# Performance work log

Measured on AMD Instinct MI355X. Metric: run time of the kernel, lower is better.

The kernel has to match this reference:

```python
import jax, jax.numpy as jnp
import numpy as np

FP8_MAX = 448.0  # torch.finfo(torch.float8_e4m3fn).max
FP8_MIN = -448.0
EPS = 1e-12


def fp8_quantize(x):
    """Scalar (per-tensor) dynamic fp8 e4m3 quantization, matching fp8_quantize(scalar=True).
    Returns fp8-rounded values (stored as float32) and the reciprocal scale (float32)."""
    amax = jnp.clip(jnp.max(jnp.abs(x)), EPS, None)
    scale = FP8_MAX / amax
    q = jnp.clip(x * scale, FP8_MIN, FP8_MAX)
    q = q.astype(jnp.float8_e4m3fn).astype(jnp.float32)  # rounding to fp8 grid
    return q, (1.0 / scale).astype(jnp.float32)


def setup_inputs() -> dict:
    key = jax.random.key(0)
    k_in, k_w, k_b = jax.random.split(key, 3)
    M, K, N = 16384, 2048, 2048
    input = jax.random.normal(k_in, (M, K), dtype=jnp.float32)
    weight = jax.random.normal(k_w, (N, K), dtype=jnp.float32) * 0.02
    # from_unquant: quantize weight once at init
    qweight, w_scale = fp8_quantize(weight)
    bias = jax.random.normal(k_b, (N,), dtype=jnp.float32) * 0.01
    return {"input": input, "qweight": qweight, "w_scale": w_scale, "bias": bias}


def reference(input, qweight, w_scale, bias):
    # dynamic per-tensor fp8 quantization of the activation
    qinput, a_scale = fp8_quantize(input)  # [M, K], scalar
    # torch._scaled_mm(qinput, qweight.t(), scale_a, scale_b, bias):
    #   out = (A_fp8 @ B_fp8) * scale_a * scale_b + bias, in out_dtype
    out = jnp.matmul(qinput, qweight.T)  # [M, N]
    out = out * (a_scale * w_scale) + bias[None, :]
    return out.astype(jnp.float32)
```

## Files before the change

### kernel.cpp

```cpp
#include <hip/hip_runtime.h>

typedef float f32x4 __attribute__((ext_vector_type(4)));
typedef int   i32x4 __attribute__((ext_vector_type(4)));
typedef int   i32x8 __attribute__((ext_vector_type(8)));

#define FP8MAX 448.0f
#define AMAX_BLOCKS 2048
#define WQ_BLOCKS 512
#define QA_BLOCKS 2048


__device__ __forceinline__ unsigned pack_fp8_exact(float4 v) {
    int r = __builtin_amdgcn_cvt_pk_fp8_f32(v.x, v.y, 0, false);
    return (unsigned)__builtin_amdgcn_cvt_pk_fp8_f32(v.z, v.w, r, true);
}

__global__ __launch_bounds__(256) void amax_and_wquant(
    const float4* __restrict__ x, float* __restrict__ partial, int n4,
    const float4* __restrict__ w, uint4* __restrict__ qw, int n16w) {
    if (blockIdx.x < AMAX_BLOCKS) {
        float m0 = 0.0f, m1 = 0.0f;
        int stride = AMAX_BLOCKS * 256;
        int i = blockIdx.x * 256 + threadIdx.x;
        for (; i + stride < n4; i += 2 * stride) {
            float4 a = x[i];
            float4 b = x[i + stride];
            m0 = fmaxf(m0, fmaxf(fmaxf(fabsf(a.x), fabsf(a.y)), fmaxf(fabsf(a.z), fabsf(a.w))));
            m1 = fmaxf(m1, fmaxf(fmaxf(fabsf(b.x), fabsf(b.y)), fmaxf(fabsf(b.z), fabsf(b.w))));
        }
        if (i < n4) {
            float4 a = x[i];
            m0 = fmaxf(m0, fmaxf(fmaxf(fabsf(a.x), fabsf(a.y)), fmaxf(fabsf(a.z), fabsf(a.w))));
        }
        float m = fmaxf(m0, m1);
#pragma unroll
        for (int off = 32; off > 0; off >>= 1)
            m = fmaxf(m, __shfl_down(m, off, 64));
        __shared__ float ws[4];
        if ((threadIdx.x & 63) == 0) ws[threadIdx.x >> 6] = m;
        __syncthreads();
        if (threadIdx.x == 0)
            partial[blockIdx.x] = fmaxf(fmaxf(ws[0], ws[1]), fmaxf(ws[2], ws[3]));
    } else {
        int stride = WQ_BLOCKS * 256;
        for (int i = (blockIdx.x - AMAX_BLOCKS) * 256 + threadIdx.x; i < n16w; i += stride) {
            uint4 r;
            r.x = pack_fp8_exact(w[i * 4 + 0]);
            r.y = pack_fp8_exact(w[i * 4 + 1]);
            r.z = pack_fp8_exact(w[i * 4 + 2]);
            r.w = pack_fp8_exact(w[i * 4 + 3]);
            qw[i] = r;
        }
    }
}


__device__ __forceinline__ float reduce_partials(const float* __restrict__ partial) {
    float m = 0.0f;
#pragma unroll
    for (int j = 0; j < AMAX_BLOCKS / 256; ++j)
        m = fmaxf(m, partial[threadIdx.x + j * 256]);
#pragma unroll
    for (int off = 32; off > 0; off >>= 1)
        m = fmaxf(m, __shfl_down(m, off, 64));
    __shared__ float ws[4];
    if ((threadIdx.x & 63) == 0) ws[threadIdx.x >> 6] = m;
    __syncthreads();
    return fmaxf(fmaxf(ws[0], ws[1]), fmaxf(ws[2], ws[3]));
}

__device__ __forceinline__ unsigned pack_fp8_clip(float4 v, float s) {
    float a = fminf(fmaxf(v.x * s, -FP8MAX), FP8MAX);
    float b = fminf(fmaxf(v.y * s, -FP8MAX), FP8MAX);
    float c = fminf(fmaxf(v.z * s, -FP8MAX), FP8MAX);
    float d = fminf(fmaxf(v.w * s, -FP8MAX), FP8MAX);
    int r = __builtin_amdgcn_cvt_pk_fp8_f32(a, b, 0, false);
    r = __builtin_amdgcn_cvt_pk_fp8_f32(c, d, r, true);
    return (unsigned)r;
}

__global__ __launch_bounds__(256) void quant_act(
    const float4* __restrict__ x, uint4* __restrict__ q,
    const float* __restrict__ partial, unsigned* __restrict__ amax_bits, int n16) {
    float amax = fmaxf(reduce_partials(partial), 1e-12f);
    if (blockIdx.x == 0 && threadIdx.x == 0)
        *amax_bits = __float_as_uint(amax);
    float s = FP8MAX / amax;
    int stride = QA_BLOCKS * 256;
    for (int i = blockIdx.x * 256 + threadIdx.x; i < n16; i += stride) {
        uint4 r;
        r.x = pack_fp8_clip(x[i * 4 + 0], s);
        r.y = pack_fp8_clip(x[i * 4 + 1], s);
        r.z = pack_fp8_clip(x[i * 4 + 2], s);
        r.w = pack_fp8_clip(x[i * 4 + 3], s);
        q[i] = r;
    }
}


__global__ __launch_bounds__(256) void gemm_fp8_mx(
    const unsigned char* __restrict__ Aq,
    const unsigned char* __restrict__ Bq,
    const unsigned* __restrict__ amax_bits,
    const float* __restrict__ w_scale_p,
    const float* __restrict__ bias,
    float* __restrict__ C,
    int M, int N, int K) {
    __shared__ unsigned char lA[128 * 128];
    __shared__ unsigned char lB[128 * 128];

    const int tid = threadIdx.x;
    const int lane = tid & 63;
    const int wave = tid >> 6;

    const int bn = blockIdx.x;
    const int bm = blockIdx.y;
    const int row0 = bm * 128;
    const int col0 = bn * 128;

    const int wm = wave >> 1;
    const int wn = wave & 1;
    const int m_base = wm * 64;
    const int n_base = wn * 64;

    const int lane_lo = lane & 15;
    const int h = lane >> 4;
    const int c0 = 2 * h;
    const int c1 = 2 * h + 1;

    f32x4 acc[4][4];
#pragma unroll
    for (int i = 0; i < 4; ++i)
#pragma unroll
        for (int j = 0; j < 4; ++j)
            acc[i][j] = (f32x4){0.f, 0.f, 0.f, 0.f};

    union frag8 { i32x8 v; i32x4 half[2]; };

    for (int k0 = 0; k0 < K; k0 += 128) {
#pragma unroll
        for (int it = 0; it < 4; ++it) {
            int chunk = tid + it * 256;
            int r = chunk >> 3;
            int cpos = chunk & 7;
            int csrc = cpos ^ (r & 7);
            const unsigned char* gA = Aq + (size_t)(row0 + r) * K + (k0 + csrc * 16);
            const unsigned char* gB = Bq + (size_t)(col0 + r) * K + (k0 + csrc * 16);
            __builtin_amdgcn_global_load_lds(
                (const __attribute__((address_space(1))) void*)gA,
                (__attribute__((address_space(3))) void*)(lA + chunk * 16), 16, 0, 0);
            __builtin_amdgcn_global_load_lds(
                (const __attribute__((address_space(1))) void*)gB,
                (__attribute__((address_space(3))) void*)(lB + chunk * 16), 16, 0, 0);
        }
        __syncthreads();

        frag8 af[4], bf[4];
#pragma unroll
        for (int i = 0; i < 4; ++i) {
            int m = m_base + i * 16 + lane_lo;
            int p0 = c0 ^ (m & 7);
            int p1 = c1 ^ (m & 7);
            af[i].half[0] = *(const i32x4*)(lA + m * 128 + p0 * 16);
            af[i].half[1] = *(const i32x4*)(lA + m * 128 + p1 * 16);
        }
#pragma unroll
        for (int j = 0; j < 4; ++j) {
            int n = n_base + j * 16 + lane_lo;
            int p0 = c0 ^ (n & 7);
            int p1 = c1 ^ (n & 7);
            bf[j].half[0] = *(const i32x4*)(lB + n * 128 + p0 * 16);
            bf[j].half[1] = *(const i32x4*)(lB + n * 128 + p1 * 16);
        }
#pragma unroll
        for (int i = 0; i < 4; ++i)
#pragma unroll
            for (int j = 0; j < 4; ++j)
                acc[i][j] = __builtin_amdgcn_mfma_scale_f32_16x16x128_f8f6f4(
                    af[i].v, bf[j].v, acc[i][j],
                    0, 0,
                    0, 0x7F7F7F7F,
                    0, 0x7F7F7F7F);
        __syncthreads();
    }

    float amax = fmaxf(__uint_as_float(*amax_bits), 1e-12f);
    float scale = FP8MAX / amax;
    float a_scale = 1.0f / scale;
    float s = a_scale * w_scale_p[0];

    const int lane_hi = lane >> 4;
#pragma unroll
    for (int i = 0; i < 4; ++i) {
#pragma unroll
        for (int j = 0; j < 4; ++j) {
            int col = col0 + n_base + j * 16 + lane_lo;
            float bv = bias[col];
#pragma unroll
            for (int r = 0; r < 4; ++r) {
                int row = row0 + m_base + i * 16 + lane_hi * 4 + r;
                C[(size_t)row * N + col] = acc[i][j][r] * s + bv;
            }
        }
    }
}


extern "C" void kernel_launch(void* const* d_in, const int* in_sizes, int n_in,
                              void* d_out, int out_size, void* d_ws, size_t ws_size,
                              hipStream_t stream) {
    const float* input   = (const float*)d_in[0];
    const float* qweight = (const float*)d_in[1];
    const float* w_scale = (const float*)d_in[2];
    const float* bias    = (const float*)d_in[3];
    float* out = (float*)d_out;

    const int N = in_sizes[3];
    const int K = in_sizes[1] / N;
    const int M = in_sizes[0] / K;

    unsigned* amax_bits = (unsigned*)d_ws;
    float* partial = (float*)((char*)d_ws + 256);
    unsigned char* qA = (unsigned char*)d_ws + 16384;
    unsigned char* qW = qA + (size_t)M * K;

    const int n4a  = (M / 4) * K;
    const int n16w = (N / 4) * K / 4;
    hipLaunchKernelGGL(amax_and_wquant, dim3(AMAX_BLOCKS + WQ_BLOCKS), dim3(256), 0, stream,
                       (const float4*)input, partial, n4a,
                       (const float4*)qweight, (uint4*)qW, n16w);

    const int n16a = n4a / 4;
    hipLaunchKernelGGL(quant_act, dim3(QA_BLOCKS), dim3(256), 0, stream,
                       (const float4*)input, (uint4*)qA, partial, amax_bits, n16a);

    hipLaunchKernelGGL(gemm_fp8_mx, dim3(N / 128, M / 128), dim3(256), 0, stream,
                       qA, qW, amax_bits, w_scale, bias, out, M, N, K);
}
```

Before: 325.7 us.

## Use 256x256 tiles with 8 waves and double-buffered LDS prefetch in FP8 GEMM

The GEMM tile grows from 128x128 with 4 waves to 256x256 with 8 waves, and each wave now computes a 128x64 sub-tile. LDS is double-buffered so the next K-tile's global-to-LDS loads are interleaved with the MFMA phases of the current tile, with barriers and s_setprio around the MFMA bursts. This aims to hide global load latency and halve the global traffic per FLOP. In exchange it raises LDS use to 128 KB per block and doubles the accumulator registers, which limits occupancy to about one block per CU.

```diff
diff --git a/kernel.cpp b/kernel.cpp
--- a/kernel.cpp
+++ b/kernel.cpp
@@ -98,7 +98,7 @@
 }
 
 
-__global__ __launch_bounds__(256) void gemm_fp8_mx(
+__global__ __launch_bounds__(512) void gemm_fp8_mx2(
     const unsigned char* __restrict__ Aq,
     const unsigned char* __restrict__ Bq,
     const unsigned* __restrict__ amax_bits,
@@ -106,8 +106,8 @@
     const float* __restrict__ bias,
     float* __restrict__ C,
     int M, int N, int K) {
-    __shared__ unsigned char lA[128 * 128];
-    __shared__ unsigned char lB[128 * 128];
+    __shared__ unsigned char lA[2][256 * 128];
+    __shared__ unsigned char lB[2][256 * 128];
 
     const int tid = threadIdx.x;
     const int lane = tid & 63;
@@ -115,12 +115,12 @@
 
     const int bn = blockIdx.x;
     const int bm = blockIdx.y;
-    const int row0 = bm * 128;
-    const int col0 = bn * 128;
-
-    const int wm = wave >> 1;
-    const int wn = wave & 1;
-    const int m_base = wm * 64;
+    const int row0 = bm * 256;
+    const int col0 = bn * 256;
+
+    const int wm = wave >> 2;
+    const int wn = wave & 3;
+    const int m_base = wm * 128;
     const int n_base = wn * 64;
 
     const int lane_lo = lane & 15;
@@ -128,60 +128,98 @@
     const int c0 = 2 * h;
     const int c1 = 2 * h + 1;
 
-    f32x4 acc[4][4];
-#pragma unroll
-    for (int i = 0; i < 4; ++i)
+    const int s_r    = tid >> 3;
+    const int s_cpos = tid & 7;
+
+    f32x4 acc[8][4];
+#pragma unroll
+    for (int i = 0; i < 8; ++i)
 #pragma unroll
         for (int j = 0; j < 4; ++j)
             acc[i][j] = (f32x4){0.f, 0.f, 0.f, 0.f};
 
     union frag8 { i32x8 v; i32x4 half[2]; };
 
-    for (int k0 = 0; k0 < K; k0 += 128) {
-#pragma unroll
-        for (int it = 0; it < 4; ++it) {
-            int chunk = tid + it * 256;
-            int r = chunk >> 3;
-            int cpos = chunk & 7;
-            int csrc = cpos ^ (r & 7);
-            const unsigned char* gA = Aq + (size_t)(row0 + r) * K + (k0 + csrc * 16);
-            const unsigned char* gB = Bq + (size_t)(col0 + r) * K + (k0 + csrc * 16);
-            __builtin_amdgcn_global_load_lds(
-                (const __attribute__((address_space(1))) void*)gA,
-                (__attribute__((address_space(3))) void*)(lA + chunk * 16), 16, 0, 0);
-            __builtin_amdgcn_global_load_lds(
-                (const __attribute__((address_space(1))) void*)gB,
-                (__attribute__((address_space(3))) void*)(lB + chunk * 16), 16, 0, 0);
-        }
-        __syncthreads();
-
-        frag8 af[4], bf[4];
-#pragma unroll
-        for (int i = 0; i < 4; ++i) {
-            int m = m_base + i * 16 + lane_lo;
-            int p0 = c0 ^ (m & 7);
-            int p1 = c1 ^ (m & 7);
-            af[i].half[0] = *(const i32x4*)(lA + m * 128 + p0 * 16);
-            af[i].half[1] = *(const i32x4*)(lA + m * 128 + p1 * 16);
-        }
-#pragma unroll
-        for (int j = 0; j < 4; ++j) {
-            int n = n_base + j * 16 + lane_lo;
-            int p0 = c0 ^ (n & 7);
-            int p1 = c1 ^ (n & 7);
-            bf[j].half[0] = *(const i32x4*)(lB + n * 128 + p0 * 16);
-            bf[j].half[1] = *(const i32x4*)(lB + n * 128 + p1 * 16);
-        }
-#pragma unroll
-        for (int i = 0; i < 4; ++i)
+#define STAGE_PAIR(BUFI, KT, IT)                                                        \
+    {                                                                                   \
+        int r_ = s_r + (IT) * 64;                                                       \
+        int csrc_ = s_cpos ^ (r_ & 7);                                                  \
+        int ldst_ = (r_ * 8 + s_cpos) * 16;                                             \
+        const unsigned char* gA_ = Aq + (size_t)(row0 + r_) * K + ((KT) * 128 + csrc_ * 16); \
+        const unsigned char* gB_ = Bq + (size_t)(col0 + r_) * K + ((KT) * 128 + csrc_ * 16); \
+        __builtin_amdgcn_global_load_lds(                                               \
+            (const __attribute__((address_space(1))) void*)gA_,                         \
+            (__attribute__((address_space(3))) void*)(&lA[BUFI][0] + ldst_), 16, 0, 0); \
+        __builtin_amdgcn_global_load_lds(                                               \
+            (const __attribute__((address_space(1))) void*)gB_,                         \
+            (__attribute__((address_space(3))) void*)(&lB[BUFI][0] + ldst_), 16, 0, 0); \
+    }
+
+#pragma unroll
+    for (int it = 0; it < 4; ++it)
+        STAGE_PAIR(0, 0, it)
+    asm volatile("s_waitcnt vmcnt(0)" ::: "memory");
+    __builtin_amdgcn_s_barrier();
+
+    const int NT = K >> 7;
+    int buf = 0;
+    for (int t = 0; t < NT; ++t) {
+        const unsigned char* cA = &lA[buf][0];
+        const unsigned char* cB = &lB[buf][0];
+        const int nbuf = buf ^ 1;
+        const bool pf = (t + 1 < NT);
+
+        frag8 bfr[4];
+#pragma unroll
+        for (int p = 0; p < 4; ++p) {
+            if (p == 0) {
+#pragma unroll
+                for (int j = 0; j < 4; ++j) {
+                    int n = n_base + j * 16 + lane_lo;
+                    int p0 = c0 ^ (n & 7);
+                    int p1 = c1 ^ (n & 7);
+                    bfr[j].half[0] = *(const i32x4*)(cB + n * 128 + p0 * 16);
+                    bfr[j].half[1] = *(const i32x4*)(cB + n * 128 + p1 * 16);
+                }
+            }
+            frag8 a0, a1;
+            {
+                int m = m_base + (2 * p) * 16 + lane_lo;
+                int p0 = c0 ^ (m & 7);
+                int p1 = c1 ^ (m & 7);
+                a0.half[0] = *(const i32x4*)(cA + m * 128 + p0 * 16);
+                a0.half[1] = *(const i32x4*)(cA + m * 128 + p1 * 16);
+            }
+            {
+                int m = m_base + (2 * p + 1) * 16 + lane_lo;
+                int p0 = c0 ^ (m & 7);
+                int p1 = c1 ^ (m & 7);
+                a1.half[0] = *(const i32x4*)(cA + m * 128 + p0 * 16);
+                a1.half[1] = *(const i32x4*)(cA + m * 128 + p1 * 16);
+            }
+            if (pf)
+                STAGE_PAIR(nbuf, t + 1, p)
+
+            __builtin_amdgcn_s_barrier();
+
+            __builtin_amdgcn_s_setprio(1);
 #pragma unroll
             for (int j = 0; j < 4; ++j)
-                acc[i][j] = __builtin_amdgcn_mfma_scale_f32_16x16x128_f8f6f4(
-                    af[i].v, bf[j].v, acc[i][j],
-                    0, 0,
-                    0, 0x7F7F7F7F,
-                    0, 0x7F7F7F7F);
-        __syncthreads();
+                acc[2 * p][j] = __builtin_amdgcn_mfma_scale_f32_16x16x128_f8f6f4(
+                    a0.v, bfr[j].v, acc[2 * p][j],
+                    0, 0, 0, 0x7F7F7F7F, 0, 0x7F7F7F7F);
+#pragma unroll
+            for (int j = 0; j < 4; ++j)
+                acc[2 * p + 1][j] = __builtin_amdgcn_mfma_scale_f32_16x16x128_f8f6f4(
+                    a1.v, bfr[j].v, acc[2 * p + 1][j],
+                    0, 0, 0, 0x7F7F7F7F, 0, 0x7F7F7F7F);
+            __builtin_amdgcn_s_setprio(0);
+
+            if (p == 3 && pf)
+                asm volatile("s_waitcnt vmcnt(0)" ::: "memory");
+            __builtin_amdgcn_s_barrier();
+        }
+        buf = nbuf;
     }
 
     float amax = fmaxf(__uint_as_float(*amax_bits), 1e-12f);
@@ -191,7 +229,7 @@
 
     const int lane_hi = lane >> 4;
 #pragma unroll
-    for (int i = 0; i < 4; ++i) {
+    for (int i = 0; i < 8; ++i) {
 #pragma unroll
         for (int j = 0; j < 4; ++j) {
             int col = col0 + n_base + j * 16 + lane_lo;
@@ -203,6 +241,7 @@
             }
         }
     }
+#undef STAGE_PAIR
 }
 
 
@@ -234,6 +273,6 @@
     hipLaunchKernelGGL(quant_act, dim3(QA_BLOCKS), dim3(256), 0, stream,
                        (const float4*)input, (uint4*)qA, partial, amax_bits, n16a);
 
-    hipLaunchKernelGGL(gemm_fp8_mx, dim3(N / 128, M / 128), dim3(256), 0, stream,
+    hipLaunchKernelGGL(gemm_fp8_mx2, dim3(N / 256, M / 256), dim3(512), 0, stream,
                        qA, qW, amax_bits, w_scale, bias, out, M, N, K);
 }
```

New measurement: 352.9 us. 1.08x slower.
